# Kernel optimization log

Hardware: AMD Instinct MI355X
Metric: run time of the kernel (lower is better)

## Reference

```python
import jax, jax.numpy as jnp
import numpy as np


def setup_inputs() -> dict:
    key = jax.random.key(0)
    ks = jax.random.split(key, 8)
    B, T, IN, H, OUT = 64, 512, 256, 1024, 256
    s_in = 1.0 / np.sqrt(IN)
    s_h = 1.0 / np.sqrt(H)
    return {
        "X": jax.random.normal(ks[0], (B, T, IN), jnp.float32),
        "Wx": jax.random.normal(ks[1], (H, IN), jnp.float32) * s_in,
        "bx": jnp.zeros((H,), jnp.float32),
        "Wh": jax.random.normal(ks[2], (H, H), jnp.float32) * s_h,
        "Uz": jax.random.normal(ks[3], (H, IN), jnp.float32) * s_in,
        "bz": jnp.zeros((H,), jnp.float32),
        "Vz": jax.random.normal(ks[4], (H, H), jnp.float32) * s_h,
        "Ur": jax.random.normal(ks[5], (H, IN), jnp.float32) * s_in,
        "br": jnp.zeros((H,), jnp.float32),
        "Vr": jax.random.normal(ks[6], (H, H), jnp.float32) * s_h,
        "Wo": jax.random.normal(ks[7], (OUT, H), jnp.float32) * s_h,
        "bo": jnp.zeros((OUT,), jnp.float32),
    }


def reference(X, Wx, bx, Wh, Uz, bz, Vz, Ur, br, Vr, Wo, bo):
    # Nonstandard GRU from philip-bl/tensor_train_rnn: gates (z, r) are
    # computed AFTER the hidden-state update, so gate values from timestep
    # t-1 modulate the update at timestep t. h, r, z all start at zero.
    B, T, _ = X.shape
    H = Wx.shape[0]
    # Batch all input projections into three big GEMMs up-front: [B,T,H]
    x_h = jnp.einsum("bti,hi->bth", X, Wx) + bx
    x_z = jnp.einsum("bti,hi->bth", X, Uz) + bz
    x_r = jnp.einsum("bti,hi->bth", X, Ur) + br

    def step(carry, inp):
        h, r, z = carry
        xh, xz, xr = inp  # each [B,H]
        h_tilde = jnp.tanh(xh + (h * r) @ Wh.T)  # tanh activation, dropout p=0 is identity
        h = z * h + (1.0 - z) * h_tilde
        z = jax.nn.sigmoid(xz + h @ Vz.T)
        r = jax.nn.sigmoid(xr + h @ Vr.T)
        return (h, r, z), None

    zeros = jnp.zeros((B, H), X.dtype)
    xs = (jnp.swapaxes(x_h, 0, 1), jnp.swapaxes(x_z, 0, 1), jnp.swapaxes(x_r, 0, 1))  # [T,B,H]
    (h, _, _), _ = jax.lax.scan(step, (zeros, zeros, zeros), xs)
    return h @ Wo.T + bo  # [B, OUT]
```

## Files before the change

### kernel.cpp

```cpp
#include <hip/hip_runtime.h>


#define BB 64
#define TT 512
#define KIN 256
#define HH 1024
#define NOUT 256

typedef float  f32x4 __attribute__((ext_vector_type(4)));
typedef short  s16x8 __attribute__((ext_vector_type(8)));
typedef unsigned int u32x4 __attribute__((ext_vector_type(4)));
typedef unsigned short u16x4 __attribute__((ext_vector_type(4)));

#define MFMA16(a, b, c) __builtin_amdgcn_mfma_f32_16x16x32_bf16((a), (b), (c), 0, 0, 0)

static __device__ __forceinline__ s16x8 as16(u32x4 v) { return __builtin_bit_cast(s16x8, v); }

static __device__ __forceinline__ unsigned short f2bf(float f) {
  unsigned u = __float_as_uint(f);
  u += 0x7FFFu + ((u >> 16) & 1u);
  return (unsigned short)(u >> 16);
}
static __device__ __forceinline__ float bf2f(unsigned short h) {
  return __uint_as_float(((unsigned)h) << 16);
}

static __device__ __forceinline__ float tanh_fast(float x) {
  float xc = fminf(fmaxf(x, -15.f), 15.f);
  float e = __expf(2.f * xc);
  return (e - 1.f) / (e + 1.f);
}
static __device__ __forceinline__ float sigmoid_fast(float x) {
  float xc = fminf(fmaxf(x, -30.f), 30.f);
  return 1.f / (1.f + __expf(-xc));
}

static __device__ __forceinline__ void st_dw(unsigned* p, unsigned v) {
  asm volatile("global_store_dword %0, %1, off sc0 sc1" :: "v"(p), "v"(v) : "memory");
}
template <int OFF>
static __device__ __forceinline__ void ld128o(u32x4& d, const unsigned* p) {
  asm volatile("global_load_dwordx4 %0, %1, off offset:%2 sc0 sc1"
               : "=v"(d) : "v"(p), "i"(OFF));
}
static __device__ __forceinline__ void tie16(u32x4& a0, u32x4& a1, u32x4& a2, u32x4& a3,
                                             u32x4& a4, u32x4& a5, u32x4& a6, u32x4& a7,
                                             u32x4& a8, u32x4& a9, u32x4& aA, u32x4& aB,
                                             u32x4& aC, u32x4& aD, u32x4& aE, u32x4& aF) {
  asm volatile("s_waitcnt vmcnt(0)"
               : "+v"(a0), "+v"(a1), "+v"(a2), "+v"(a3),
                 "+v"(a4), "+v"(a5), "+v"(a6), "+v"(a7),
                 "+v"(a8), "+v"(a9), "+v"(aA), "+v"(aB),
                 "+v"(aC), "+v"(aD), "+v"(aE), "+v"(aF)
               :: "memory");
}

static __device__ __forceinline__ unsigned pk(unsigned hi, unsigned lo) {
  return __builtin_amdgcn_perm(hi, lo, 0x07060302u);
}
static __device__ __forceinline__ u32x4 pack_frag(u32x4 a, u32x4 b) {
  u32x4 r;
  r.x = pk(a.y, a.x); r.y = pk(a.w, a.z);
  r.z = pk(b.y, b.x); r.w = pk(b.w, b.z);
  return r;
}

static __device__ __forceinline__ void load_validated(
    const unsigned* rp0, unsigned tag, bool& dead, u32x4 (&a)[8]) {
  const unsigned* p1 = rp0 + 1024;
  const unsigned* p2 = rp0 + 2048;
  const unsigned* p3 = rp0 + 3072;
  u32x4 r0, r1, r2, r3, r4, r5, r6, r7, r8, r9, rA, rB, rC, rD, rE, rF;
  int guard = 0;
  while (true) {
    ld128o<0>(r0, rp0); ld128o<1024>(r1, rp0); ld128o<2048>(r2, rp0); ld128o<3072>(r3, rp0);
    ld128o<0>(r4, p1);  ld128o<1024>(r5, p1);  ld128o<2048>(r6, p1);  ld128o<3072>(r7, p1);
    ld128o<0>(r8, p2);  ld128o<1024>(r9, p2);  ld128o<2048>(rA, p2);  ld128o<3072>(rB, p2);
    ld128o<0>(rC, p3);  ld128o<1024>(rD, p3);  ld128o<2048>(rE, p3);  ld128o<3072>(rF, p3);
    tie16(r0, r1, r2, r3, r4, r5, r6, r7, r8, r9, rA, rB, rC, rD, rE, rF);
    unsigned bad = 0;
#define CHK(R) bad |= (R.x ^ tag) | (R.y ^ tag) | (R.z ^ tag) | (R.w ^ tag)
    CHK(r0); CHK(r1); CHK(r2); CHK(r3); CHK(r4); CHK(r5); CHK(r6); CHK(r7);
    CHK(r8); CHK(r9); CHK(rA); CHK(rB); CHK(rC); CHK(rD); CHK(rE); CHK(rF);
#undef CHK
    bad &= 0xFFFFu;
    if (__all(bad == 0)) break;
    if (dead || ++guard > 4096) { dead = true; break; }
    if (guard > 1) {
      if (guard < 6) __builtin_amdgcn_s_sleep(2);
      else           __builtin_amdgcn_s_sleep(4);
    }
  }
  a[0] = pack_frag(r0, r1); a[1] = pack_frag(r2, r3);
  a[2] = pack_frag(r4, r5); a[3] = pack_frag(r6, r7);
  a[4] = pack_frag(r8, r9); a[5] = pack_frag(rA, rB);
  a[6] = pack_frag(rC, rD); a[7] = pack_frag(rE, rF);
}

static constexpr size_t SZ_XP   = (size_t)TT * BB * HH * 2;
static constexpr size_t OFF_XH  = 0;
static constexpr size_t OFF_XZ  = OFF_XH + SZ_XP;
static constexpr size_t OFF_XR  = OFF_XZ + SZ_XP;
static constexpr size_t OFF_XB  = OFF_XR + SZ_XP;
static constexpr size_t OFF_WHP = OFF_XB + (size_t)BB * TT * KIN * 2;
static constexpr size_t OFF_VZP = OFF_WHP + (size_t)HH * HH * 2;
static constexpr size_t OFF_VRP = OFF_VZP + (size_t)HH * HH * 2;
static constexpr size_t OFF_WXP = OFF_VRP + (size_t)HH * HH * 2;
static constexpr size_t OFF_UZP = OFF_WXP + (size_t)HH * KIN * 2;
static constexpr size_t OFF_URP = OFF_UZP + (size_t)HH * KIN * 2;
static constexpr size_t OFF_HB  = OFF_URP + (size_t)HH * KIN * 2;
static constexpr size_t OFF_HRB = OFF_HB + (size_t)4 * 16 * HH * 4;
static constexpr size_t OFF_HF  = OFF_HRB + (size_t)4 * 16 * HH * 4;

__global__ void __launch_bounds__(256) k_convert_x(const float* __restrict__ X,
                                                   unsigned short* __restrict__ Xb) {
  size_t i = ((size_t)blockIdx.x * 256 + threadIdx.x) * 4;
  f32x4 v = *(const f32x4*)(X + i);
  u16x4 o = { f2bf(v[0]), f2bf(v[1]), f2bf(v[2]), f2bf(v[3]) };
  *(u16x4*)(Xb + i) = o;
}

__global__ void __launch_bounds__(256) k_pack_w(
    const float* __restrict__ Wh, const float* __restrict__ Vz, const float* __restrict__ Vr,
    const float* __restrict__ Wx, const float* __restrict__ Uz, const float* __restrict__ Ur,
    unsigned short* __restrict__ Whp, unsigned short* __restrict__ Vzp, unsigned short* __restrict__ Vrp,
    unsigned short* __restrict__ Wxp, unsigned short* __restrict__ Uzp, unsigned short* __restrict__ Urp) {
  int z = blockIdx.y;
  const float* src; unsigned short* dst; int K;
  switch (z) {
    case 0: src = Wh; dst = Whp; K = 1024; break;
    case 1: src = Vz; dst = Vzp; K = 1024; break;
    case 2: src = Vr; dst = Vrp; K = 1024; break;
    case 3: src = Wx; dst = Wxp; K = 256;  break;
    case 4: src = Uz; dst = Uzp; K = 256;  break;
    default: src = Ur; dst = Urp; K = 256; break;
  }
  int KK = K >> 5;
  int total = 64 * KK * 64;
  int tau = blockIdx.x * 256 + threadIdx.x;
  if (tau >= total) return;
  int lane = tau & 63;
  int kk = (tau >> 6) % KK;
  int ct = tau / (KK * 64);
  int q = lane >> 4, cl = lane & 15;
  const float* s = src + (size_t)(ct * 16 + cl) * K + kk * 32 + q * 8;
  f32x4 v0 = *(const f32x4*)s;
  f32x4 v1 = *(const f32x4*)(s + 4);
  u32x4 o;
  o.x = (unsigned)f2bf(v0[0]) | ((unsigned)f2bf(v0[1]) << 16);
  o.y = (unsigned)f2bf(v0[2]) | ((unsigned)f2bf(v0[3]) << 16);
  o.z = (unsigned)f2bf(v1[0]) | ((unsigned)f2bf(v1[1]) << 16);
  o.w = (unsigned)f2bf(v1[2]) | ((unsigned)f2bf(v1[3]) << 16);
  *(u32x4*)(dst + (size_t)tau * 8) = o;
}

__global__ void __launch_bounds__(256) k_proj(
    const unsigned short* __restrict__ Xb,
    const unsigned short* __restrict__ Wxp, const unsigned short* __restrict__ Uzp,
    const unsigned short* __restrict__ Urp,
    const float* __restrict__ bx, const float* __restrict__ bz, const float* __restrict__ br,
    unsigned short* __restrict__ XH, unsigned short* __restrict__ XZ, unsigned short* __restrict__ XR) {
  __shared__ u32x4 As[4 * 8 * 64];
  const int tid = threadIdx.x;
  const int mb = blockIdx.x, cb = blockIdx.y, mu = blockIdx.z;

#pragma unroll
  for (int i = 0; i < 8; ++i) {
    int fid = i * 256 + tid;
    int lane = fid & 63, kk = (fid >> 6) & 7, rt = fid >> 9;
    int q = lane >> 4, cl = lane & 15;
    int mrow = mb * 64 + rt * 16 + cl;
    As[fid] = *(const u32x4*)(Xb + (size_t)mrow * KIN + kk * 32 + q * 8);
  }
  __syncthreads();

  const int lane = tid & 63, w = tid >> 6;
  const int q = lane >> 4, cl = lane & 15;
  const unsigned short* Bp = (mu == 0) ? Wxp : (mu == 1) ? Uzp : Urp;
  const float* bias        = (mu == 0) ? bx  : (mu == 1) ? bz  : br;
  unsigned short* Dst      = (mu == 0) ? XH  : (mu == 1) ? XZ  : XR;

  f32x4 z4 = {0.f, 0.f, 0.f, 0.f};
  f32x4 acc[4] = {z4, z4, z4, z4};
  const int ctg = cb * 4 + w;
#pragma unroll
  for (int kk = 0; kk < 8; ++kk) {
    u32x4 b = *(const u32x4*)(Bp + ((size_t)(ctg * 8 + kk) * 64 + lane) * 8);
#pragma unroll
    for (int rt = 0; rt < 4; ++rt)
      acc[rt] = MFMA16(as16(As[(rt * 8 + kk) * 64 + lane]), as16(b), acc[rt]);
  }
  const int col = cb * 64 + w * 16 + cl;
  const float bv = bias[col];
#pragma unroll
  for (int rt = 0; rt < 4; ++rt) {
#pragma unroll
    for (int j = 0; j < 4; ++j) {
      int m = mb * 64 + rt * 16 + q * 4 + j;
      int t = m & (TT - 1), b = m >> 9;
      Dst[((size_t)t * BB + b) * HH + col] = f2bf(acc[rt][j] + bv);
    }
  }
}

__global__ void __launch_bounds__(256, 1) k_scan(
    const unsigned short* __restrict__ XH, const unsigned short* __restrict__ XZ,
    const unsigned short* __restrict__ XR,
    const unsigned short* __restrict__ Whp, const unsigned short* __restrict__ Vzp,
    const unsigned short* __restrict__ Vrp,
    unsigned* __restrict__ hb32all, unsigned* __restrict__ hrb32all,
    float* __restrict__ hfinal) {
  __shared__ f32x4 redA[16 * 64];
  __shared__ f32x4 redB[16 * 64];
  __shared__ f32x4 redC[16 * 64];

  const int tid = threadIdx.x;
  const int lane = tid & 63, w = tid >> 6;
  const int q = lane >> 4, cl = lane & 15;
  const int blk = blockIdx.x;
  const int g = blk >> 4, c = blk & 15;
  const int c4 = c * 4, kw = w * 8;

  unsigned* hb  = hb32all  + (size_t)g * 16 * HH;
  unsigned* hrb = hrb32all + (size_t)g * 16 * HH;

  u32x4 wh[4][8], vz[4][8];
#pragma unroll
  for (int ct = 0; ct < 4; ++ct)
#pragma unroll
    for (int k = 0; k < 8; ++k) {
      size_t fi = (((size_t)(c4 + ct) * 32 + kw + k) * 64 + lane) * 8;
      wh[ct][k] = *(const u32x4*)(Whp + fi);
      vz[ct][k] = *(const u32x4*)(Vzp + fi);
    }

  const int hcol = c * 64 + w * 16 + cl;
  const int brow0 = g * 16 + q * 4;

  const unsigned* rpA = hrb + w * 4096 + lane * 4;
  const unsigned* rpB = hb  + w * 4096 + lane * 4;
  const unsigned C = (unsigned)hcol;
  const unsigned sbase = ((C >> 8) * 8 + ((C >> 5) & 7)) * 512 + ((C >> 2) & 1) * 256 +
                         (((C >> 3) & 3) * 16 + q * 4) * 4 + (C & 3);
  unsigned* spA = hb  + sbase;
  unsigned* spB = hrb + sbase;

  const f32x4 z4 = {0.f, 0.f, 0.f, 0.f};
  f32x4 hreg = z4, zreg = z4;
  unsigned short xz_u[4] = {0, 0, 0, 0};
  bool dead = false;

  for (int t = 0; t < TT; ++t) {
    unsigned short xh_u[4];
#pragma unroll
    for (int j = 0; j < 4; ++j)
      xh_u[j] = XH[((size_t)t * BB + brow0 + j) * HH + hcol];

    f32x4 acc[4] = {z4, z4, z4, z4};
    if (t > 0) {
      u32x4 a[8];
      load_validated(rpA, (unsigned)t, dead, a);
#pragma unroll
      for (int k = 0; k < 8; ++k) {
        s16x8 av = as16(a[k]);
#pragma unroll
        for (int ct = 0; ct < 4; ++ct)
          acc[ct] = MFMA16(av, as16(wh[ct][k]), acc[ct]);
      }
    }
#pragma unroll
    for (int ct = 0; ct < 4; ++ct) redA[(w * 4 + ct) * 64 + lane] = acc[ct];
    __syncthreads();
    f32x4 S = redA[(0 * 4 + w) * 64 + lane];
    S += redA[(1 * 4 + w) * 64 + lane];
    S += redA[(2 * 4 + w) * 64 + lane];
    S += redA[(3 * 4 + w) * 64 + lane];

    if (t > 0) {
      f32x4 Sz = redB[(0 * 4 + w) * 64 + lane];
      Sz += redB[(1 * 4 + w) * 64 + lane];
      Sz += redB[(2 * 4 + w) * 64 + lane];
      Sz += redB[(3 * 4 + w) * 64 + lane];
#pragma unroll
      for (int j = 0; j < 4; ++j)
        zreg[j] = sigmoid_fast(Sz[j] + bf2f(xz_u[j]));
    }

    float hn[4];
#pragma unroll
    for (int j = 0; j < 4; ++j) {
      float pre = S[j] + bf2f(xh_u[j]);
      float ht = tanh_fast(pre);
      hn[j] = zreg[j] * hreg[j] + (1.f - zreg[j]) * ht;
      hreg[j] = hn[j];
    }
    if (t == TT - 1) break;

    const unsigned tagn = (unsigned)(t + 1);
#pragma unroll
    for (int j = 0; j < 4; ++j)
      st_dw(spA + j * 4, ((unsigned)f2bf(hn[j]) << 16) | tagn);

    unsigned short xr_u[4];
#pragma unroll
    for (int j = 0; j < 4; ++j) {
      xz_u[j] = XZ[((size_t)t * BB + brow0 + j) * HH + hcol];
      xr_u[j] = XR[((size_t)t * BB + brow0 + j) * HH + hcol];
    }
    u32x4 vr0[8];
#pragma unroll
    for (int k = 0; k < 8; ++k)
      vr0[k] = *(const u32x4*)(Vrp + (((size_t)(c4 + 0) * 32 + kw + k) * 64 + lane) * 8);

    u32x4 b[8];
    load_validated(rpB, tagn, dead, b);

    f32x4 ar[4] = {z4, z4, z4, z4};
#pragma unroll
    for (int k = 0; k < 8; ++k)
      ar[0] = MFMA16(as16(b[k]), as16(vr0[k]), ar[0]);
#pragma unroll
    for (int ct = 1; ct < 4; ++ct) {
      u32x4 vrk[8];
#pragma unroll
      for (int k = 0; k < 8; ++k)
        vrk[k] = *(const u32x4*)(Vrp + (((size_t)(c4 + ct) * 32 + kw + k) * 64 + lane) * 8);
#pragma unroll
      for (int k = 0; k < 8; ++k)
        ar[ct] = MFMA16(as16(b[k]), as16(vrk[k]), ar[ct]);
    }
#pragma unroll
    for (int ct = 0; ct < 4; ++ct) redC[(w * 4 + ct) * 64 + lane] = ar[ct];
    __syncthreads();
    f32x4 Sr = redC[(0 * 4 + w) * 64 + lane];
    Sr += redC[(1 * 4 + w) * 64 + lane];
    Sr += redC[(2 * 4 + w) * 64 + lane];
    Sr += redC[(3 * 4 + w) * 64 + lane];

    float rh[4];
#pragma unroll
    for (int j = 0; j < 4; ++j) {
      float rv = sigmoid_fast(Sr[j] + bf2f(xr_u[j]));
      rh[j] = rv * hreg[j];
    }
#pragma unroll
    for (int j = 0; j < 4; ++j)
      st_dw(spB + j * 4, ((unsigned)f2bf(rh[j]) << 16) | tagn);

    f32x4 az[4] = {z4, z4, z4, z4};
#pragma unroll
    for (int ct = 0; ct < 4; ++ct)
#pragma unroll
      for (int k = 0; k < 8; ++k)
        az[ct] = MFMA16(as16(b[k]), as16(vz[ct][k]), az[ct]);
#pragma unroll
    for (int ct = 0; ct < 4; ++ct) redB[(w * 4 + ct) * 64 + lane] = az[ct];
  }

#pragma unroll
  for (int j = 0; j < 4; ++j)
    hfinal[(size_t)(brow0 + j) * HH + hcol] = hreg[j];
}

__global__ void __launch_bounds__(256) k_out(const float* __restrict__ hf,
                                             const float* __restrict__ Wo,
                                             const float* __restrict__ bo,
                                             float* __restrict__ out) {
  __shared__ float hs[HH];
  const int b = blockIdx.x, tid = threadIdx.x;
  *(f32x4*)&hs[tid * 4] = *(const f32x4*)(hf + (size_t)b * HH + tid * 4);
  __syncthreads();
  float acc = bo[tid];
  const f32x4* wr = (const f32x4*)(Wo + (size_t)tid * HH);
#pragma unroll 8
  for (int k = 0; k < HH / 4; ++k) {
    f32x4 wv = wr[k];
    f32x4 hv = *(const f32x4*)&hs[k * 4];
    acc += wv[0] * hv[0] + wv[1] * hv[1] + wv[2] * hv[2] + wv[3] * hv[3];
  }
  out[(size_t)b * NOUT + tid] = acc;
}

extern "C" void kernel_launch(void* const* d_in, const int* in_sizes, int n_in,
                              void* d_out, int out_size, void* d_ws, size_t ws_size,
                              hipStream_t stream) {
  (void)in_sizes; (void)n_in; (void)out_size; (void)ws_size;
  const float* X  = (const float*)d_in[0];
  const float* Wx = (const float*)d_in[1];
  const float* bx = (const float*)d_in[2];
  const float* Wh = (const float*)d_in[3];
  const float* Uz = (const float*)d_in[4];
  const float* bz = (const float*)d_in[5];
  const float* Vz = (const float*)d_in[6];
  const float* Ur = (const float*)d_in[7];
  const float* br = (const float*)d_in[8];
  const float* Vr = (const float*)d_in[9];
  const float* Wo = (const float*)d_in[10];
  const float* bo = (const float*)d_in[11];

  char* ws = (char*)d_ws;
  unsigned short* XHp = (unsigned short*)(ws + OFF_XH);
  unsigned short* XZp = (unsigned short*)(ws + OFF_XZ);
  unsigned short* XRp = (unsigned short*)(ws + OFF_XR);
  unsigned short* Xb  = (unsigned short*)(ws + OFF_XB);
  unsigned short* Whp = (unsigned short*)(ws + OFF_WHP);
  unsigned short* Vzp = (unsigned short*)(ws + OFF_VZP);
  unsigned short* Vrp = (unsigned short*)(ws + OFF_VRP);
  unsigned short* Wxp = (unsigned short*)(ws + OFF_WXP);
  unsigned short* Uzp = (unsigned short*)(ws + OFF_UZP);
  unsigned short* Urp = (unsigned short*)(ws + OFF_URP);
  unsigned* hbp  = (unsigned*)(ws + OFF_HB);
  unsigned* hrbp = (unsigned*)(ws + OFF_HRB);
  float* hfp = (float*)(ws + OFF_HF);

  k_convert_x<<<8192, 256, 0, stream>>>(X, Xb);
  k_pack_w<<<dim3(512, 6), 256, 0, stream>>>(Wh, Vz, Vr, Wx, Uz, Ur,
                                             Whp, Vzp, Vrp, Wxp, Uzp, Urp);
  k_proj<<<dim3(512, 16, 3), 256, 0, stream>>>(Xb, Wxp, Uzp, Urp, bx, bz, br,
                                               XHp, XZp, XRp);
  k_scan<<<64, 256, 0, stream>>>(XHp, XZp, XRp, Whp, Vzp, Vrp,
                                 hbp, hrbp, hfp);
  k_out<<<64, 256, 0, stream>>>(hfp, Wo, bo, (float*)d_out);
}
```

Baseline: 3.790 ms.

## Split validated flag-polling loads into halves and overlap MFMAs with second-half arrival

The 16 tagged loads of the cross-block hidden state are now split into two halves. The code waits only on the first half (vmcnt(8)), validates it and starts the MFMAs on it while the second half is still in flight, and falls back to a polling loop only when the tags are stale. The z-gate reduction is moved ahead of the h-loads so its latency is hidden, and a __syncthreads is added after the redB write to guard the reordered read. This is meant to hide global-memory latency on the serial recurrence critical path. The cost is more code, higher register pressure, and one extra barrier per timestep.

New measurement: 3.387 ms. 1.12x faster.

```diff
diff --git a/kernel.cpp b/kernel.cpp
--- a/kernel.cpp
+++ b/kernel.cpp
@@ -43,17 +43,20 @@
   asm volatile("global_load_dwordx4 %0, %1, off offset:%2 sc0 sc1"
                : "=v"(d) : "v"(p), "i"(OFF));
 }
-static __device__ __forceinline__ void tie16(u32x4& a0, u32x4& a1, u32x4& a2, u32x4& a3,
-                                             u32x4& a4, u32x4& a5, u32x4& a6, u32x4& a7,
-                                             u32x4& a8, u32x4& a9, u32x4& aA, u32x4& aB,
-                                             u32x4& aC, u32x4& aD, u32x4& aE, u32x4& aF) {
+static __device__ __forceinline__ void tie8_vm8(u32x4& a0, u32x4& a1, u32x4& a2, u32x4& a3,
+                                                u32x4& a4, u32x4& a5, u32x4& a6, u32x4& a7) {
+  asm volatile("s_waitcnt vmcnt(8)"
+               : "+v"(a0), "+v"(a1), "+v"(a2), "+v"(a3),
+                 "+v"(a4), "+v"(a5), "+v"(a6), "+v"(a7) :: "memory");
+}
+static __device__ __forceinline__ void tie8_vm0(u32x4& a0, u32x4& a1, u32x4& a2, u32x4& a3,
+                                                u32x4& a4, u32x4& a5, u32x4& a6, u32x4& a7) {
   asm volatile("s_waitcnt vmcnt(0)"
                : "+v"(a0), "+v"(a1), "+v"(a2), "+v"(a3),
-                 "+v"(a4), "+v"(a5), "+v"(a6), "+v"(a7),
-                 "+v"(a8), "+v"(a9), "+v"(aA), "+v"(aB),
-                 "+v"(aC), "+v"(aD), "+v"(aE), "+v"(aF)
-               :: "memory");
-}
+                 "+v"(a4), "+v"(a5), "+v"(a6), "+v"(a7) :: "memory");
+}
+
+#define CHK4(R) (((R).x ^ tag) | ((R).y ^ tag) | ((R).z ^ tag) | ((R).w ^ tag))
 
 static __device__ __forceinline__ unsigned pk(unsigned hi, unsigned lo) {
   return __builtin_amdgcn_perm(hi, lo, 0x07060302u);
@@ -65,25 +68,17 @@
   return r;
 }
 
-static __device__ __forceinline__ void load_validated(
-    const unsigned* rp0, unsigned tag, bool& dead, u32x4 (&a)[8]) {
-  const unsigned* p1 = rp0 + 1024;
-  const unsigned* p2 = rp0 + 2048;
-  const unsigned* p3 = rp0 + 3072;
-  u32x4 r0, r1, r2, r3, r4, r5, r6, r7, r8, r9, rA, rB, rC, rD, rE, rF;
+static __device__ __forceinline__ void poll8(
+    const unsigned* pa, const unsigned* pb, unsigned tag, bool& dead,
+    u32x4& r0, u32x4& r1, u32x4& r2, u32x4& r3,
+    u32x4& r4, u32x4& r5, u32x4& r6, u32x4& r7) {
   int guard = 0;
   while (true) {
-    ld128o<0>(r0, rp0); ld128o<1024>(r1, rp0); ld128o<2048>(r2, rp0); ld128o<3072>(r3, rp0);
-    ld128o<0>(r4, p1);  ld128o<1024>(r5, p1);  ld128o<2048>(r6, p1);  ld128o<3072>(r7, p1);
-    ld128o<0>(r8, p2);  ld128o<1024>(r9, p2);  ld128o<2048>(rA, p2);  ld128o<3072>(rB, p2);
-    ld128o<0>(rC, p3);  ld128o<1024>(rD, p3);  ld128o<2048>(rE, p3);  ld128o<3072>(rF, p3);
-    tie16(r0, r1, r2, r3, r4, r5, r6, r7, r8, r9, rA, rB, rC, rD, rE, rF);
-    unsigned bad = 0;
-#define CHK(R) bad |= (R.x ^ tag) | (R.y ^ tag) | (R.z ^ tag) | (R.w ^ tag)
-    CHK(r0); CHK(r1); CHK(r2); CHK(r3); CHK(r4); CHK(r5); CHK(r6); CHK(r7);
-    CHK(r8); CHK(r9); CHK(rA); CHK(rB); CHK(rC); CHK(rD); CHK(rE); CHK(rF);
-#undef CHK
-    bad &= 0xFFFFu;
+    ld128o<0>(r0, pa); ld128o<1024>(r1, pa); ld128o<2048>(r2, pa); ld128o<3072>(r3, pa);
+    ld128o<0>(r4, pb); ld128o<1024>(r5, pb); ld128o<2048>(r6, pb); ld128o<3072>(r7, pb);
+    tie8_vm0(r0, r1, r2, r3, r4, r5, r6, r7);
+    unsigned bad = (CHK4(r0) | CHK4(r1) | CHK4(r2) | CHK4(r3) |
+                    CHK4(r4) | CHK4(r5) | CHK4(r6) | CHK4(r7)) & 0xFFFFu;
     if (__all(bad == 0)) break;
     if (dead || ++guard > 4096) { dead = true; break; }
     if (guard > 1) {
@@ -91,10 +86,6 @@
       else           __builtin_amdgcn_s_sleep(4);
     }
   }
-  a[0] = pack_frag(r0, r1); a[1] = pack_frag(r2, r3);
-  a[2] = pack_frag(r4, r5); a[3] = pack_frag(r6, r7);
-  a[4] = pack_frag(r8, r9); a[5] = pack_frag(rA, rB);
-  a[6] = pack_frag(rC, rD); a[7] = pack_frag(rE, rF);
 }
 
 static constexpr size_t SZ_XP   = (size_t)TT * BB * HH * 2;
@@ -256,16 +247,58 @@
     for (int j = 0; j < 4; ++j)
       xh_u[j] = XH[((size_t)t * BB + brow0 + j) * HH + hcol];
 
+    if (t > 0) {
+      f32x4 Sz = redB[(0 * 4 + w) * 64 + lane];
+      Sz += redB[(1 * 4 + w) * 64 + lane];
+      Sz += redB[(2 * 4 + w) * 64 + lane];
+      Sz += redB[(3 * 4 + w) * 64 + lane];
+#pragma unroll
+      for (int j = 0; j < 4; ++j)
+        zreg[j] = sigmoid_fast(Sz[j] + bf2f(xz_u[j]));
+    }
+
     f32x4 acc[4] = {z4, z4, z4, z4};
     if (t > 0) {
-      u32x4 a[8];
-      load_validated(rpA, (unsigned)t, dead, a);
-#pragma unroll
-      for (int k = 0; k < 8; ++k) {
-        s16x8 av = as16(a[k]);
+      const unsigned tag = (unsigned)t;
+      const unsigned* p1 = rpA + 1024;
+      const unsigned* p2 = rpA + 2048;
+      const unsigned* p3 = rpA + 3072;
+      u32x4 r0, r1, r2, r3, r4, r5, r6, r7, r8, r9, rA_, rB_, rC_, rD_, rE_, rF_;
+      ld128o<0>(r0, rpA); ld128o<1024>(r1, rpA); ld128o<2048>(r2, rpA); ld128o<3072>(r3, rpA);
+      ld128o<0>(r4, p1);  ld128o<1024>(r5, p1);  ld128o<2048>(r6, p1);  ld128o<3072>(r7, p1);
+      ld128o<0>(r8, p2);  ld128o<1024>(r9, p2);  ld128o<2048>(rA_, p2); ld128o<3072>(rB_, p2);
+      ld128o<0>(rC_, p3); ld128o<1024>(rD_, p3); ld128o<2048>(rE_, p3); ld128o<3072>(rF_, p3);
+      tie8_vm8(r0, r1, r2, r3, r4, r5, r6, r7);
+      unsigned bad0 = (CHK4(r0) | CHK4(r1) | CHK4(r2) | CHK4(r3) |
+                       CHK4(r4) | CHK4(r5) | CHK4(r6) | CHK4(r7)) & 0xFFFFu;
+      if (!__all(bad0 == 0)) {
+        tie8_vm0(r8, r9, rA_, rB_, rC_, rD_, rE_, rF_);
+        poll8(rpA, p1, tag, dead, r0, r1, r2, r3, r4, r5, r6, r7);
+      }
+      u32x4 ah[4];
+      ah[0] = pack_frag(r0, r1); ah[1] = pack_frag(r2, r3);
+      ah[2] = pack_frag(r4, r5); ah[3] = pack_frag(r6, r7);
+#pragma unroll
+      for (int k = 0; k < 4; ++k) {
+        s16x8 av = as16(ah[k]);
 #pragma unroll
         for (int ct = 0; ct < 4; ++ct)
           acc[ct] = MFMA16(av, as16(wh[ct][k]), acc[ct]);
+      }
+      tie8_vm0(r8, r9, rA_, rB_, rC_, rD_, rE_, rF_);
+      unsigned bad1 = (CHK4(r8) | CHK4(r9) | CHK4(rA_) | CHK4(rB_) |
+                       CHK4(rC_) | CHK4(rD_) | CHK4(rE_) | CHK4(rF_)) & 0xFFFFu;
+      if (!__all(bad1 == 0))
+        poll8(p2, p3, tag, dead, r8, r9, rA_, rB_, rC_, rD_, rE_, rF_);
+      u32x4 al[4];
+      al[0] = pack_frag(r8, r9);  al[1] = pack_frag(rA_, rB_);
+      al[2] = pack_frag(rC_, rD_); al[3] = pack_frag(rE_, rF_);
+#pragma unroll
+      for (int k = 0; k < 4; ++k) {
+        s16x8 av = as16(al[k]);
+#pragma unroll
+        for (int ct = 0; ct < 4; ++ct)
+          acc[ct] = MFMA16(av, as16(wh[ct][k + 4]), acc[ct]);
       }
     }
 #pragma unroll
@@ -276,16 +309,6 @@
     S += redA[(2 * 4 + w) * 64 + lane];
     S += redA[(3 * 4 + w) * 64 + lane];
 
-    if (t > 0) {
-      f32x4 Sz = redB[(0 * 4 + w) * 64 + lane];
-      Sz += redB[(1 * 4 + w) * 64 + lane];
-      Sz += redB[(2 * 4 + w) * 64 + lane];
-      Sz += redB[(3 * 4 + w) * 64 + lane];
-#pragma unroll
-      for (int j = 0; j < 4; ++j)
-        zreg[j] = sigmoid_fast(Sz[j] + bf2f(xz_u[j]));
-    }
-
     float hn[4];
 #pragma unroll
     for (int j = 0; j < 4; ++j) {
@@ -307,27 +330,67 @@
       xz_u[j] = XZ[((size_t)t * BB + brow0 + j) * HH + hcol];
       xr_u[j] = XR[((size_t)t * BB + brow0 + j) * HH + hcol];
     }
-    u32x4 vr0[8];
-#pragma unroll
-    for (int k = 0; k < 8; ++k)
-      vr0[k] = *(const u32x4*)(Vrp + (((size_t)(c4 + 0) * 32 + kw + k) * 64 + lane) * 8);
-
-    u32x4 b[8];
-    load_validated(rpB, tagn, dead, b);
-
+    u32x4 vr00[4], vr01[4];
+#pragma unroll
+    for (int k = 0; k < 4; ++k) {
+      vr00[k] = *(const u32x4*)(Vrp + (((size_t)(c4 + 0) * 32 + kw + k) * 64 + lane) * 8);
+      vr01[k] = *(const u32x4*)(Vrp + (((size_t)(c4 + 0) * 32 + kw + k + 4) * 64 + lane) * 8);
+    }
+
+    u32x4 bh[4], bl[4];
     f32x4 ar[4] = {z4, z4, z4, z4};
-#pragma unroll
-    for (int k = 0; k < 8; ++k)
-      ar[0] = MFMA16(as16(b[k]), as16(vr0[k]), ar[0]);
-#pragma unroll
-    for (int ct = 1; ct < 4; ++ct) {
-      u32x4 vrk[8];
-#pragma unroll
-      for (int k = 0; k < 8; ++k)
-        vrk[k] = *(const u32x4*)(Vrp + (((size_t)(c4 + ct) * 32 + kw + k) * 64 + lane) * 8);
-#pragma unroll
-      for (int k = 0; k < 8; ++k)
-        ar[ct] = MFMA16(as16(b[k]), as16(vrk[k]), ar[ct]);
+    {
+      const unsigned tag = tagn;
+      const unsigned* p1 = rpB + 1024;
+      const unsigned* p2 = rpB + 2048;
+      const unsigned* p3 = rpB + 3072;
+      u32x4 r0, r1, r2, r3, r4, r5, r6, r7, r8, r9, rA_, rB_, rC_, rD_, rE_, rF_;
+      ld128o<0>(r0, rpB); ld128o<1024>(r1, rpB); ld128o<2048>(r2, rpB); ld128o<3072>(r3, rpB);
+      ld128o<0>(r4, p1);  ld128o<1024>(r5, p1);  ld128o<2048>(r6, p1);  ld128o<3072>(r7, p1);
+      ld128o<0>(r8, p2);  ld128o<1024>(r9, p2);  ld128o<2048>(rA_, p2); ld128o<3072>(rB_, p2);
+      ld128o<0>(rC_, p3); ld128o<1024>(rD_, p3); ld128o<2048>(rE_, p3); ld128o<3072>(rF_, p3);
+      tie8_vm8(r0, r1, r2, r3, r4, r5, r6, r7);
+      unsigned bad0 = (CHK4(r0) | CHK4(r1) | CHK4(r2) | CHK4(r3) |
+                       CHK4(r4) | CHK4(r5) | CHK4(r6) | CHK4(r7)) & 0xFFFFu;
+      if (!__all(bad0 == 0)) {
+        tie8_vm0(r8, r9, rA_, rB_, rC_, rD_, rE_, rF_);
+        poll8(rpB, p1, tag, dead, r0, r1, r2, r3, r4, r5, r6, r7);
+      }
+      bh[0] = pack_frag(r0, r1); bh[1] = pack_frag(r2, r3);
+      bh[2] = pack_frag(r4, r5); bh[3] = pack_frag(r6, r7);
+#pragma unroll
+      for (int k = 0; k < 4; ++k)
+        ar[0] = MFMA16(as16(bh[k]), as16(vr00[k]), ar[0]);
+#pragma unroll
+      for (int ct = 1; ct < 4; ++ct) {
+        u32x4 vrk[4];
+#pragma unroll
+        for (int k = 0; k < 4; ++k)
+          vrk[k] = *(const u32x4*)(Vrp + (((size_t)(c4 + ct) * 32 + kw + k) * 64 + lane) * 8);
+#pragma unroll
+        for (int k = 0; k < 4; ++k)
+          ar[ct] = MFMA16(as16(bh[k]), as16(vrk[k]), ar[ct]);
+      }
+      tie8_vm0(r8, r9, rA_, rB_, rC_, rD_, rE_, rF_);
+      unsigned bad1 = (CHK4(r8) | CHK4(r9) | CHK4(rA_) | CHK4(rB_) |
+                       CHK4(rC_) | CHK4(rD_) | CHK4(rE_) | CHK4(rF_)) & 0xFFFFu;
+      if (!__all(bad1 == 0))
+        poll8(p2, p3, tag, dead, r8, r9, rA_, rB_, rC_, rD_, rE_, rF_);
+      bl[0] = pack_frag(r8, r9);  bl[1] = pack_frag(rA_, rB_);
+      bl[2] = pack_frag(rC_, rD_); bl[3] = pack_frag(rE_, rF_);
+#pragma unroll
+      for (int k = 0; k < 4; ++k)
+        ar[0] = MFMA16(as16(bl[k]), as16(vr01[k]), ar[0]);
+#pragma unroll
+      for (int ct = 1; ct < 4; ++ct) {
+        u32x4 vrk[4];
+#pragma unroll
+        for (int k = 0; k < 4; ++k)
+          vrk[k] = *(const u32x4*)(Vrp + (((size_t)(c4 + ct) * 32 + kw + k + 4) * 64 + lane) * 8);
+#pragma unroll
+        for (int k = 0; k < 4; ++k)
+          ar[ct] = MFMA16(as16(bl[k]), as16(vrk[k]), ar[ct]);
+      }
     }
 #pragma unroll
     for (int ct = 0; ct < 4; ++ct) redC[(w * 4 + ct) * 64 + lane] = ar[ct];
@@ -349,12 +412,17 @@
 
     f32x4 az[4] = {z4, z4, z4, z4};
 #pragma unroll
-    for (int ct = 0; ct < 4; ++ct)
-#pragma unroll
-      for (int k = 0; k < 8; ++k)
-        az[ct] = MFMA16(as16(b[k]), as16(vz[ct][k]), az[ct]);
+    for (int ct = 0; ct < 4; ++ct) {
+#pragma unroll
+      for (int k = 0; k < 4; ++k)
+        az[ct] = MFMA16(as16(bh[k]), as16(vz[ct][k]), az[ct]);
+#pragma unroll
+      for (int k = 0; k < 4; ++k)
+        az[ct] = MFMA16(as16(bl[k]), as16(vz[ct][k + 4]), az[ct]);
+    }
 #pragma unroll
     for (int ct = 0; ct < 4; ++ct) redB[(w * 4 + ct) * 64 + lane] = az[ct];
+    __syncthreads();
   }
 
 #pragma unroll
```
